# Kernel optimization log

Measured on AMD Instinct MI355X. Metric: run time of the kernel, lower is better.

The kernel has to match this reference:

```python
import jax, jax.numpy as jnp
import numpy as np

D_MODEL = 1024
NUM_HEADS = 16
HEAD_DIM = D_MODEL // NUM_HEADS
THETA = 10000.0


def _rope(x, cos, sin):
    # x: [B, H, S, hd]; cos/sin: [S, hd//2] (broadcast over B, H)
    x_even = x[..., 0::2]
    x_odd = x[..., 1::2]
    y_even = x_even * cos - x_odd * sin
    y_odd = x_even * sin + x_odd * cos
    # interleave back: stack on last dim then flatten
    y = jnp.stack((y_even, y_odd), axis=-1)
    return y.reshape(x.shape)


def setup_inputs() -> dict:
    key = jax.random.key(0)
    ks = jax.random.split(key, 5)
    B, S = 2, 2048
    x = jax.random.normal(ks[0], (B, S, D_MODEL), dtype=jnp.float32)
    scale = 1.0 / np.sqrt(D_MODEL)
    Wq = jax.random.normal(ks[1], (D_MODEL, D_MODEL), dtype=jnp.float32) * scale
    Wk = jax.random.normal(ks[2], (D_MODEL, D_MODEL), dtype=jnp.float32) * scale
    Wv = jax.random.normal(ks[3], (D_MODEL, D_MODEL), dtype=jnp.float32) * scale
    Wo = jax.random.normal(ks[4], (D_MODEL, D_MODEL), dtype=jnp.float32) * scale
    token_positions = jnp.arange(S, dtype=jnp.int64 if jax.config.jax_enable_x64 else jnp.int32)
    return {"x": x, "token_positions": token_positions, "Wq": Wq, "Wk": Wk, "Wv": Wv, "Wo": Wo}


def reference(x, token_positions, Wq, Wk, Wv, Wo):
    B, S, _ = x.shape
    # nn.Linear(d,d,bias=False): y = x @ W.T
    q = (x @ Wq.T).reshape(B, S, NUM_HEADS, HEAD_DIM).transpose(0, 2, 1, 3)
    k = (x @ Wk.T).reshape(B, S, NUM_HEADS, HEAD_DIM).transpose(0, 2, 1, 3)
    v = (x @ Wv.T).reshape(B, S, NUM_HEADS, HEAD_DIM).transpose(0, 2, 1, 3)

    # RoPE tables gathered at token_positions
    freqs = 1.0 / THETA ** (jnp.arange(0, HEAD_DIM, 2, dtype=jnp.float32) / HEAD_DIM)
    angles = token_positions.astype(jnp.float32)[:, None] * freqs[None, :]  # [S, hd//2]
    cos, sin = jnp.cos(angles), jnp.sin(angles)
    q = _rope(q, cos, sin)
    k = _rope(k, cos, sin)

    scores = jnp.einsum("bhqd,bhkd->bhqk", q, k) / np.sqrt(HEAD_DIM)
    causal = jnp.tril(jnp.ones((S, S), dtype=bool))
    scores = jnp.where(causal, scores, jnp.finfo(scores.dtype).min)
    attn = jax.nn.softmax(scores, axis=-1)
    out = jnp.einsum("bhqk,bhkd->bhqd", attn, v)  # [B,H,S,hd]
    out = out.transpose(0, 2, 1, 3).reshape(B, S, D_MODEL)
    return out @ Wo.T
```

## Files before the change

kernel.cpp:

```cpp
#include <hip/hip_runtime.h>

#define S_LEN 2048
#define NH 16
#define HD 64
#define DM 1024
#define MTOT 4096

#define QSCALE 0.18033688011112042f

typedef short bf16x8 __attribute__((ext_vector_type(8)));
typedef float f32x4 __attribute__((ext_vector_type(4)));
typedef unsigned short u16x8 __attribute__((ext_vector_type(8)));
typedef int i32x4 __attribute__((ext_vector_type(4)));

__device__ __forceinline__ unsigned short f2bf(float f) {
  unsigned int u = __builtin_bit_cast(unsigned int, f);
  u += 0x7fffu + ((u >> 16) & 1u);
  return (unsigned short)(u >> 16);
}

__device__ __forceinline__ unsigned int cvt_pk_bf16(float lo, float hi) {
  unsigned int r;
  asm("v_cvt_pk_bf16_f32 %0, %1, %2" : "=v"(r) : "v"(lo), "v"(hi));
  return r;
}

__device__ __forceinline__ void async_copy16(const void* g, void* l) {
  __builtin_amdgcn_global_load_lds(
      (const __attribute__((address_space(1))) unsigned int*)g,
      (__attribute__((address_space(3))) unsigned int*)l, 16, 0, 0);
}

__global__ void cvt_bf16_kernel(const float* __restrict__ src,
                                unsigned short* __restrict__ dst, int n) {
  int i = (blockIdx.x * 256 + threadIdx.x) * 8;
  if (i >= n) return;
  const float4* s = (const float4*)(src + i);
  float4 v0 = s[0], v1 = s[1];
  u16x8 o;
  o[0] = f2bf(v0.x); o[1] = f2bf(v0.y); o[2] = f2bf(v0.z); o[3] = f2bf(v0.w);
  o[4] = f2bf(v1.x); o[5] = f2bf(v1.y); o[6] = f2bf(v1.z); o[7] = f2bf(v1.w);
  *(u16x8*)(dst + i) = o;
}

__global__ void cvt_w_kernel(const float* __restrict__ w0, const float* __restrict__ w1,
                             const float* __restrict__ w2, const float* __restrict__ w3,
                             unsigned short* __restrict__ dst) {
  int z = blockIdx.y;
  const float* src = (z == 0) ? w0 : (z == 1) ? w1 : (z == 2) ? w2 : w3;
  int i = (blockIdx.x * 256 + threadIdx.x) * 8;
  const float4* s = (const float4*)(src + i);
  float4 v0 = s[0], v1 = s[1];
  u16x8 o;
  o[0] = f2bf(v0.x); o[1] = f2bf(v0.y); o[2] = f2bf(v0.z); o[3] = f2bf(v0.w);
  o[4] = f2bf(v1.x); o[5] = f2bf(v1.y); o[6] = f2bf(v1.z); o[7] = f2bf(v1.w);
  *(u16x8*)(dst + (size_t)z * DM * DM + i) = o;
}

__global__ void sincos_tab_kernel(const int* __restrict__ pos, float2* __restrict__ tab) {
  int idx = blockIdx.x * 256 + threadIdx.x;
  int s = idx >> 5, i = idx & 31;
  float fr = expf(-(float)i * 0.28782313662425574f);
  float ang = (float)pos[s] * fr;
  float sn, cs;
  sincosf(ang, &sn, &cs);
  tab[idx] = make_float2(cs, sn);
}

__device__ __forceinline__ void gemm_core(const unsigned short* __restrict__ A,
                                          const unsigned short* __restrict__ Bt,
                                          int m0, int n0, int K,
                                          char* a_lds, char* b_lds,
                                          f32x4 (&acc)[4][4]) {
  const int tid = threadIdx.x;
  const int w = tid >> 6, l = tid & 63;
  const int wr = w >> 1, wc = w & 1;
  const int c = l & 15, g = l >> 4;

  const size_t rs = (size_t)K * 2;
  const int lr = l >> 3;
  const int jsw = ((l & 7) ^ lr) << 4;
  const char* srcA = (const char*)A + ((size_t)m0 + w * 8 + lr) * rs + jsw;
  const char* srcB = (const char*)Bt + ((size_t)n0 + w * 8 + lr) * rs + jsw;
  char* dstA = a_lds + w * 1024 + l * 16;
  char* dstB = b_lds + w * 1024 + l * 16;
  const int csw = (c & 7) << 4;
  const int nsteps = K / 64;

  auto stage = [&](int buf, int kt) {
    const int off = buf * 16384;
#pragma unroll
    for (int i = 0; i < 4; ++i) {
      async_copy16(srcA + (size_t)i * 32 * rs + kt * 128, dstA + off + i * 4096);
      async_copy16(srcB + (size_t)i * 32 * rs + kt * 128, dstB + off + i * 4096);
    }
  };

  stage(0, 0);
  asm volatile("s_waitcnt vmcnt(0)" ::: "memory");
  __syncthreads();
  int cur = 0;

  for (int kt = 0; kt < nsteps; ++kt) {
    if (kt + 1 < nsteps) stage(cur ^ 1, kt + 1);
    const char* al = a_lds + cur * 16384;
    const char* bl = b_lds + cur * 16384;
    __builtin_amdgcn_s_setprio(1);
#pragma unroll
    for (int kk = 0; kk < 2; ++kk) {
      bf16x8 af[4], bfv[4];
#pragma unroll
      for (int mi = 0; mi < 4; ++mi)
        af[mi] = *(const bf16x8*)(al + (wr * 64 + mi * 16 + c) * 128 + ((kk * 64 + g * 16) ^ csw));
#pragma unroll
      for (int ni = 0; ni < 4; ++ni)
        bfv[ni] = *(const bf16x8*)(bl + (wc * 64 + ni * 16 + c) * 128 + ((kk * 64 + g * 16) ^ csw));
#pragma unroll
      for (int mi = 0; mi < 4; ++mi)
#pragma unroll
        for (int ni = 0; ni < 4; ++ni)
          acc[mi][ni] = __builtin_amdgcn_mfma_f32_16x16x32_bf16(af[mi], bfv[ni], acc[mi][ni], 0, 0, 0);
    }
    __builtin_amdgcn_s_setprio(0);
    asm volatile("s_waitcnt vmcnt(0)" ::: "memory");
    __syncthreads();
    cur ^= 1;
  }
}

__global__ __launch_bounds__(256)
void gemm_qkv_kernel(const unsigned short* __restrict__ X,
                     const unsigned short* __restrict__ Wq,
                     const unsigned short* __restrict__ Wk,
                     const unsigned short* __restrict__ Wv,
                     const float2* __restrict__ tab,
                     unsigned short* __restrict__ Qb,
                     unsigned short* __restrict__ Kb,
                     unsigned short* __restrict__ Vt) {
  __shared__ char a_lds[2 * 16384];
  __shared__ char b_lds[2 * 16384];
  const int z = blockIdx.z;
  const unsigned short* Bt = (z == 0) ? Wq : (z == 1) ? Wk : Wv;
  const int m0 = blockIdx.x * 128, n0 = blockIdx.y * 128;

  f32x4 acc[4][4] = {};
  gemm_core(X, Bt, m0, n0, DM, a_lds, b_lds, acc);

  const int tid = threadIdx.x;
  const int w = tid >> 6, l = tid & 63;
  const int wr = w >> 1, wc = w & 1;
  const int c = l & 15, g = l >> 4;

  if (z == 2) {
#pragma unroll
    for (int mi = 0; mi < 4; ++mi)
#pragma unroll
      for (int ni = 0; ni < 4; ++ni)
#pragma unroll
        for (int r = 0; r < 4; ++r) {
          int row = m0 + wr * 64 + mi * 16 + 4 * g + r;
          int col = n0 + wc * 64 + ni * 16 + c;
          int b = row >> 11, s = row & 2047;
          int h = col >> 6, d = col & 63;
          Vt[((size_t)(b * NH + h) * HD + d) * S_LEN + s] = f2bf(acc[mi][ni][r]);
        }
  } else {
    unsigned short* QK = z ? Kb : Qb;
    const float oscale = z ? 1.0f : QSCALE;
#pragma unroll
    for (int mi = 0; mi < 4; ++mi)
#pragma unroll
      for (int ni = 0; ni < 4; ++ni) {
        int col = n0 + wc * 64 + ni * 16 + c;
        int fi = (col >> 1) & 31;
        float sgn = (col & 1) ? 1.0f : -1.0f;
#pragma unroll
        for (int r = 0; r < 4; ++r) {
          int row = m0 + wr * 64 + mi * 16 + 4 * g + r;
          int b = row >> 11, s = row & 2047;
          float v = acc[mi][ni][r];
          float p = __shfl_xor(v, 1);
          float2 csn = tab[(s << 5) | fi];
          float vr = (v * csn.x + sgn * p * csn.y) * oscale;
          int h = col >> 6, d = col & 63;
          QK[((size_t)(b * NH + h) * S_LEN + s) * HD + d] = f2bf(vr);
        }
      }
  }
}

__global__ __launch_bounds__(256)
void gemm_out_kernel(const unsigned short* __restrict__ A,
                     const unsigned short* __restrict__ Wo,
                     float* __restrict__ out) {
  __shared__ char a_lds[2 * 16384];
  __shared__ char b_lds[2 * 16384];
  const int m0 = blockIdx.x * 128, n0 = blockIdx.y * 128;
  f32x4 acc[4][4] = {};
  gemm_core(A, Wo, m0, n0, DM, a_lds, b_lds, acc);

  const int tid = threadIdx.x;
  const int w = tid >> 6, l = tid & 63;
  const int wr = w >> 1, wc = w & 1;
  const int c = l & 15, g = l >> 4;
#pragma unroll
  for (int mi = 0; mi < 4; ++mi)
#pragma unroll
    for (int ni = 0; ni < 4; ++ni)
#pragma unroll
      for (int r = 0; r < 4; ++r) {
        int row = m0 + wr * 64 + mi * 16 + 4 * g + r;
        int col = n0 + wc * 64 + ni * 16 + c;
        out[(size_t)row * DM + col] = acc[mi][ni][r];
      }
}

__global__ __launch_bounds__(256, 4)
void attn_kernel(const unsigned short* __restrict__ Q,
                 const unsigned short* __restrict__ Kb,
                 const unsigned short* __restrict__ Vt,
                 unsigned short* __restrict__ Ob) {
  __shared__ char kbuf[2][8192];
  __shared__ char vbuf[2][8192];
  const int tid = threadIdx.x;
  const int w = tid >> 6, l = tid & 63;
  const int g = l >> 4, c = l & 15;

  const unsigned int id = blockIdx.x;
  const int bh = id & 31;
  const int j = id >> 5;
  const int a = j & 7, kk = j >> 3;
  const int qblk = (kk == 0) ? a : (kk == 1) ? (15 - a) : (kk == 2) ? (16 + a) : (31 - a);
  const int q0 = qblk * 64;

  const size_t base = (size_t)bh * (S_LEN * HD);
  const char* Kc = (const char*)(Kb + base);
  const char* Vc = (const char*)(Vt + base);

  const int lr = l >> 3;
  const int jsw = ((l & 7) << 4) ^ (lr << 4);
  const int r0 = w * 8 + lr;
  const int r1 = (4 + w) * 8 + lr;
  const char* ksrc0 = Kc + r0 * 128 + jsw;
  const char* ksrc1 = Kc + r1 * 128 + jsw;
  const char* vsrc0 = Vc + r0 * 4096 + jsw;
  const char* vsrc1 = Vc + r1 * 4096 + jsw;

  bf16x8 qf0, qf1;
  {
    const unsigned short* qp = Q + base + (size_t)(q0 + w * 16 + c) * HD + g * 8;
    qf0 = *(const bf16x8*)qp;
    qf1 = *(const bf16x8*)(qp + 32);
  }
  f32x4 oacc[4] = {};
  float rsum = 0.f;
  const int csw = (c & 7) << 4;
  const int srcA = (l & 15) | ((l & 16) << 1);
  const int srcB = srcA + 16;
  const bool hi = (l >= 32);

  auto stage = [&](int buf, int t) {
    char* kd = &kbuf[buf][w * 1024 + l * 16];
    char* vd = &vbuf[buf][w * 1024 + l * 16];
    size_t ko = (size_t)t * 8192;
    size_t vo = (size_t)t * 128;
    async_copy16(ksrc0 + ko, kd);
    async_copy16(ksrc1 + ko, kd + 4096);
    async_copy16(vsrc0 + vo, vd);
    async_copy16(vsrc1 + vo, vd + 4096);
  };

  stage(0, 0);
  asm volatile("s_waitcnt vmcnt(0)" ::: "memory");
  __syncthreads();
  int cur = 0;

  for (int t = 0; t <= qblk; ++t) {
    if (t + 1 <= qblk) stage(cur ^ 1, t + 1);
    const char* kl = kbuf[cur];
    const char* vl = vbuf[cur];
    const int kv0 = t * 64;

    f32x4 sc[4] = {};
    __builtin_amdgcn_s_setprio(1);
#pragma unroll
    for (int nt = 0; nt < 4; ++nt) {
      bf16x8 k0 = *(const bf16x8*)(kl + (nt * 16 + c) * 128 + ((g * 16) ^ csw));
      bf16x8 k1 = *(const bf16x8*)(kl + (nt * 16 + c) * 128 + ((64 + g * 16) ^ csw));
      sc[nt] = __builtin_amdgcn_mfma_f32_16x16x32_bf16(k0, qf0, sc[nt], 0, 0, 0);
      sc[nt] = __builtin_amdgcn_mfma_f32_16x16x32_bf16(k1, qf1, sc[nt], 0, 0, 0);
    }
    __builtin_amdgcn_s_setprio(0);

    if (t == qblk) {
      const int qi = q0 + w * 16 + c;
#pragma unroll
      for (int nt = 0; nt < 4; ++nt)
#pragma unroll
        for (int r = 0; r < 4; ++r) {
          int kvi = kv0 + nt * 16 + 4 * g + r;
          sc[nt][r] = exp2f((kvi > qi) ? -1e30f : sc[nt][r]);
        }
    } else {
#pragma unroll
      for (int nt = 0; nt < 4; ++nt)
#pragma unroll
        for (int r = 0; r < 4; ++r)
          sc[nt][r] = exp2f(sc[nt][r]);
    }
    unsigned int pk[4][2];
#pragma unroll
    for (int nt = 0; nt < 4; ++nt) {
      rsum += (sc[nt][0] + sc[nt][1]) + (sc[nt][2] + sc[nt][3]);
      pk[nt][0] = cvt_pk_bf16(sc[nt][0], sc[nt][1]);
      pk[nt][1] = cvt_pk_bf16(sc[nt][2], sc[nt][3]);
    }

    __builtin_amdgcn_s_setprio(1);
#pragma unroll
    for (int ks = 0; ks < 2; ++ks) {
      int a0 = __shfl((int)pk[2 * ks][0], srcA);
      int a1 = __shfl((int)pk[2 * ks][1], srcA);
      int a2 = __shfl((int)pk[2 * ks][0], srcB);
      int a3 = __shfl((int)pk[2 * ks][1], srcB);
      int b0 = __shfl((int)pk[2 * ks + 1][0], srcA);
      int b1 = __shfl((int)pk[2 * ks + 1][1], srcA);
      int b2 = __shfl((int)pk[2 * ks + 1][0], srcB);
      int b3 = __shfl((int)pk[2 * ks + 1][1], srcB);
      i32x4 pw;
      pw[0] = hi ? b0 : a0;
      pw[1] = hi ? b1 : a1;
      pw[2] = hi ? b2 : a2;
      pw[3] = hi ? b3 : a3;
      bf16x8 pf = __builtin_bit_cast(bf16x8, pw);
#pragma unroll
      for (int nt = 0; nt < 4; ++nt) {
        bf16x8 vf = *(const bf16x8*)(vl + (nt * 16 + c) * 128 + ((ks * 64 + g * 16) ^ csw));
        oacc[nt] = __builtin_amdgcn_mfma_f32_16x16x32_bf16(vf, pf, oacc[nt], 0, 0, 0);
      }
    }
    __builtin_amdgcn_s_setprio(0);

    asm volatile("s_waitcnt vmcnt(0)" ::: "memory");
    __syncthreads();
    cur ^= 1;
  }

  rsum += __shfl_xor(rsum, 16);
  rsum += __shfl_xor(rsum, 32);
  const float inv = 1.0f / rsum;

  const int b = bh >> 4, h = bh & 15;
  unsigned short* dst = Ob + ((size_t)b * S_LEN + q0 + w * 16 + c) * DM + h * HD + 4 * g;
#pragma unroll
  for (int nt = 0; nt < 4; ++nt) {
    unsigned int w0 = (unsigned int)f2bf(oacc[nt][0] * inv) | ((unsigned int)f2bf(oacc[nt][1] * inv) << 16);
    unsigned int w1 = (unsigned int)f2bf(oacc[nt][2] * inv) | ((unsigned int)f2bf(oacc[nt][3] * inv) << 16);
    uint2 pr;
    pr.x = w0;
    pr.y = w1;
    *(uint2*)(dst + nt * 16) = pr;
  }
}

extern "C" void kernel_launch(void* const* d_in, const int* in_sizes, int n_in,
                              void* d_out, int out_size, void* d_ws, size_t ws_size,
                              hipStream_t stream) {
  const float* x = (const float*)d_in[0];
  const int* tpos = (const int*)d_in[1];
  const float* wq = (const float*)d_in[2];
  const float* wk = (const float*)d_in[3];
  const float* wv = (const float*)d_in[4];
  const float* wo = (const float*)d_in[5];
  float* out = (float*)d_out;

  char* ws = (char*)d_ws;
  unsigned short* xb = (unsigned short*)(ws);
  unsigned short* wqb = (unsigned short*)(ws + 8388608);
  unsigned short* wkb = wqb + DM * DM;
  unsigned short* wvb = wqb + 2 * DM * DM;
  unsigned short* wob = wqb + 3 * DM * DM;
  unsigned short* qb = (unsigned short*)(ws + 16777216);
  unsigned short* kb = (unsigned short*)(ws + 16777216 + 8388608);
  unsigned short* vt = (unsigned short*)(ws + 16777216 + 2 * 8388608);
  unsigned short* ab = (unsigned short*)(ws + 16777216 + 3 * 8388608);
  float2* tab = (float2*)(ws + 50331648);

  cvt_bf16_kernel<<<2048, 256, 0, stream>>>(x, xb, MTOT * DM);
  cvt_w_kernel<<<dim3(512, 4), 256, 0, stream>>>(wq, wk, wv, wo, wqb);
  sincos_tab_kernel<<<256, 256, 0, stream>>>(tpos, tab);

  gemm_qkv_kernel<<<dim3(32, 8, 3), 256, 0, stream>>>(xb, wqb, wkb, wvb, tab, qb, kb, vt);
  attn_kernel<<<1024, 256, 0, stream>>>(qb, kb, vt, ab);
  gemm_out_kernel<<<dim3(32, 8), 256, 0, stream>>>(ab, wob, out);
}
```

Baseline: 127.8 us.

## Pair complementary causal query blocks per attention workgroup for balanced work

Each attention workgroup now handles two query blocks, j and 31-j, back to back, so every block walks a fixed 33 KV tiles. This balances the triangular causal workload and halves the grid to 512 blocks. The output of the first block is written mid-loop, and the K/V prefetch pipeline carries on across the switch to the second block. Launch bounds drop to 2 blocks per CU, which frees registers but lowers occupancy and leaves fewer, longer blocks.

Result: no change. 128.4 us (median of 3 runs) (+0.5%).

```diff
diff --git a/kernel.cpp b/kernel.cpp
--- a/kernel.cpp
+++ b/kernel.cpp
@@ -215,7 +215,7 @@
       }
 }
 
-__global__ __launch_bounds__(256, 4)
+__global__ __launch_bounds__(256, 2)
 void attn_kernel(const unsigned short* __restrict__ Q,
                  const unsigned short* __restrict__ Kb,
                  const unsigned short* __restrict__ Vt,
@@ -229,9 +229,7 @@
   const unsigned int id = blockIdx.x;
   const int bh = id & 31;
   const int j = id >> 5;
-  const int a = j & 7, kk = j >> 3;
-  const int qblk = (kk == 0) ? a : (kk == 1) ? (15 - a) : (kk == 2) ? (16 + a) : (31 - a);
-  const int q0 = qblk * 64;
+  const int qa = j, qb = 31 - j;
 
   const size_t base = (size_t)bh * (S_LEN * HD);
   const char* Kc = (const char*)(Kb + base);
@@ -246,9 +244,15 @@
   const char* vsrc0 = Vc + r0 * 4096 + jsw;
   const char* vsrc1 = Vc + r1 * 4096 + jsw;
 
+  const unsigned short* Qrow = Q + base + (size_t)(w * 16 + c) * HD + g * 8;
+  const int b = bh >> 4, h = bh & 15;
+  unsigned short* Obase = Ob + ((size_t)b * S_LEN + w * 16 + c) * DM + h * HD + 4 * g;
+
+  int q0 = qa * 64;
+  int qcur = qa;
   bf16x8 qf0, qf1;
   {
-    const unsigned short* qp = Q + base + (size_t)(q0 + w * 16 + c) * HD + g * 8;
+    const unsigned short* qp = Qrow + (size_t)q0 * HD;
     qf0 = *(const bf16x8*)qp;
     qf1 = *(const bf16x8*)(qp + 32);
   }
@@ -274,12 +278,14 @@
   asm volatile("s_waitcnt vmcnt(0)" ::: "memory");
   __syncthreads();
   int cur = 0;
-
-  for (int t = 0; t <= qblk; ++t) {
-    if (t + 1 <= qblk) stage(cur ^ 1, t + 1);
+  int t = 0;
+
+  for (int s = 0; s < 33; ++s) {
+    if (s < 32) stage(cur ^ 1, (t == qcur) ? 0 : t + 1);
     const char* kl = kbuf[cur];
     const char* vl = vbuf[cur];
     const int kv0 = t * 64;
+    const bool last = (t == qcur);
 
     f32x4 sc[4] = {};
     __builtin_amdgcn_s_setprio(1);
@@ -292,7 +298,7 @@
     }
     __builtin_amdgcn_s_setprio(0);
 
-    if (t == qblk) {
+    if (last) {
       const int qi = q0 + w * 16 + c;
 #pragma unroll
       for (int nt = 0; nt < 4; ++nt)
@@ -341,25 +347,38 @@
     }
     __builtin_amdgcn_s_setprio(0);
 
+    if (last) {
+      float rs = rsum;
+      rs += __shfl_xor(rs, 16);
+      rs += __shfl_xor(rs, 32);
+      const float inv = 1.0f / rs;
+      unsigned short* dst = Obase + (size_t)q0 * DM;
+#pragma unroll
+      for (int nt = 0; nt < 4; ++nt) {
+        unsigned int w0 = (unsigned int)f2bf(oacc[nt][0] * inv) | ((unsigned int)f2bf(oacc[nt][1] * inv) << 16);
+        unsigned int w1 = (unsigned int)f2bf(oacc[nt][2] * inv) | ((unsigned int)f2bf(oacc[nt][3] * inv) << 16);
+        uint2 pr;
+        pr.x = w0;
+        pr.y = w1;
+        *(uint2*)(dst + nt * 16) = pr;
+        oacc[nt] = f32x4{0.f, 0.f, 0.f, 0.f};
+      }
+      rsum = 0.f;
+      if (s < 32) {
+        q0 = qb * 64;
+        qcur = qb;
+        t = 0;
+        const unsigned short* qp = Qrow + (size_t)q0 * HD;
+        qf0 = *(const bf16x8*)qp;
+        qf1 = *(const bf16x8*)(qp + 32);
+      }
+    } else {
+      ++t;
+    }
+
     asm volatile("s_waitcnt vmcnt(0)" ::: "memory");
     __syncthreads();
     cur ^= 1;
-  }
-
-  rsum += __shfl_xor(rsum, 16);
-  rsum += __shfl_xor(rsum, 32);
-  const float inv = 1.0f / rsum;
-
-  const int b = bh >> 4, h = bh & 15;
-  unsigned short* dst = Ob + ((size_t)b * S_LEN + q0 + w * 16 + c) * DM + h * HD + 4 * g;
-#pragma unroll
-  for (int nt = 0; nt < 4; ++nt) {
-    unsigned int w0 = (unsigned int)f2bf(oacc[nt][0] * inv) | ((unsigned int)f2bf(oacc[nt][1] * inv) << 16);
-    unsigned int w1 = (unsigned int)f2bf(oacc[nt][2] * inv) | ((unsigned int)f2bf(oacc[nt][3] * inv) << 16);
-    uint2 pr;
-    pr.x = w0;
-    pr.y = w1;
-    *(uint2*)(dst + nt * 16) = pr;
   }
 }
 
@@ -391,6 +410,6 @@
   sincos_tab_kernel<<<256, 256, 0, stream>>>(tpos, tab);
 
   gemm_qkv_kernel<<<dim3(32, 8, 3), 256, 0, stream>>>(xb, wqb, wkb, wvb, tab, qb, kb, vt);
-  attn_kernel<<<1024, 256, 0, stream>>>(qb, kb, vt, ab);
+  attn_kernel<<<512, 256, 0, stream>>>(qb, kb, vt, ab);
   gemm_out_kernel<<<dim3(32, 8), 256, 0, stream>>>(ab, wob, out);
 }
```

## Pair causal query blocks per workgroup and split KV tiles across two wave groups

Applied to the files above, without the earlier changes.

The attention kernel now runs 512-thread blocks, each handling a complementary pair of query blocks (j and 31-j), so every block does the same 33 KV tiles and causal load imbalance goes away. Two wave groups take alternating KV tiles with separate double-buffered LDS, and their partial outputs and row sums are merged through LDS at the end. The risks are doubled LDS use per block, fewer blocks in flight, and extra syncs and reduction work at the epilogue.

Result: faster. 123.3 us (-3.5%).

```diff
diff --git a/kernel.cpp b/kernel.cpp
--- a/kernel.cpp
+++ b/kernel.cpp
@@ -215,23 +215,23 @@
       }
 }
 
-__global__ __launch_bounds__(256, 4)
+__global__ __launch_bounds__(512, 4)
 void attn_kernel(const unsigned short* __restrict__ Q,
                  const unsigned short* __restrict__ Kb,
                  const unsigned short* __restrict__ Vt,
                  unsigned short* __restrict__ Ob) {
-  __shared__ char kbuf[2][8192];
-  __shared__ char vbuf[2][8192];
+  __shared__ char kbuf[2][2][8192];
+  __shared__ char vbuf[2][2][8192];
   const int tid = threadIdx.x;
   const int w = tid >> 6, l = tid & 63;
+  const int G = w >> 2, ws = w & 3;
   const int g = l >> 4, c = l & 15;
 
   const unsigned int id = blockIdx.x;
   const int bh = id & 31;
   const int j = id >> 5;
-  const int a = j & 7, kk = j >> 3;
-  const int qblk = (kk == 0) ? a : (kk == 1) ? (15 - a) : (kk == 2) ? (16 + a) : (31 - a);
-  const int q0 = qblk * 64;
+  const int qa = j, qb = 31 - j;
+  const int q0a = qa * 64, q0b = qb * 64;
 
   const size_t base = (size_t)bh * (S_LEN * HD);
   const char* Kc = (const char*)(Kb + base);
@@ -239,29 +239,32 @@
 
   const int lr = l >> 3;
   const int jsw = ((l & 7) << 4) ^ (lr << 4);
-  const int r0 = w * 8 + lr;
-  const int r1 = (4 + w) * 8 + lr;
-  const char* ksrc0 = Kc + r0 * 128 + jsw;
-  const char* ksrc1 = Kc + r1 * 128 + jsw;
-  const char* vsrc0 = Vc + r0 * 4096 + jsw;
-  const char* vsrc1 = Vc + r1 * 4096 + jsw;
-
-  bf16x8 qf0, qf1;
+  const int rr0 = ws * 8 + lr;
+  const int rr1 = (4 + ws) * 8 + lr;
+  const char* ksrc0 = Kc + rr0 * 128 + jsw;
+  const char* ksrc1 = Kc + rr1 * 128 + jsw;
+  const char* vsrc0 = Vc + rr0 * 4096 + jsw;
+  const char* vsrc1 = Vc + rr1 * 4096 + jsw;
+
+  bf16x8 qfA0, qfA1, qfB0, qfB1;
   {
-    const unsigned short* qp = Q + base + (size_t)(q0 + w * 16 + c) * HD + g * 8;
-    qf0 = *(const bf16x8*)qp;
-    qf1 = *(const bf16x8*)(qp + 32);
-  }
-  f32x4 oacc[4] = {};
-  float rsum = 0.f;
+    const unsigned short* qpA = Q + base + (size_t)(q0a + ws * 16 + c) * HD + g * 8;
+    qfA0 = *(const bf16x8*)qpA;
+    qfA1 = *(const bf16x8*)(qpA + 32);
+    const unsigned short* qpB = Q + base + (size_t)(q0b + ws * 16 + c) * HD + g * 8;
+    qfB0 = *(const bf16x8*)qpB;
+    qfB1 = *(const bf16x8*)(qpB + 32);
+  }
+  f32x4 oaccA[4] = {}, oaccB[4] = {};
+  float rsA = 0.f, rsB = 0.f;
   const int csw = (c & 7) << 4;
   const int srcA = (l & 15) | ((l & 16) << 1);
   const int srcB = srcA + 16;
   const bool hi = (l >= 32);
 
   auto stage = [&](int buf, int t) {
-    char* kd = &kbuf[buf][w * 1024 + l * 16];
-    char* vd = &vbuf[buf][w * 1024 + l * 16];
+    char* kd = &kbuf[G][buf][ws * 1024 + l * 16];
+    char* vd = &vbuf[G][buf][ws * 1024 + l * 16];
     size_t ko = (size_t)t * 8192;
     size_t vo = (size_t)t * 128;
     async_copy16(ksrc0 + ko, kd);
@@ -270,30 +273,21 @@
     async_copy16(vsrc1 + vo, vd + 4096);
   };
 
-  stage(0, 0);
-  asm volatile("s_waitcnt vmcnt(0)" ::: "memory");
-  __syncthreads();
-  int cur = 0;
-
-  for (int t = 0; t <= qblk; ++t) {
-    if (t + 1 <= qblk) stage(cur ^ 1, t + 1);
-    const char* kl = kbuf[cur];
-    const char* vl = vbuf[cur];
+  auto body = [&](const char* kl, const char* vl, int q0, int qcur, int t,
+                  bf16x8 q0f, bf16x8 q1f, f32x4(&oacc)[4], float& rsum) {
     const int kv0 = t * 64;
-
     f32x4 sc[4] = {};
     __builtin_amdgcn_s_setprio(1);
 #pragma unroll
     for (int nt = 0; nt < 4; ++nt) {
       bf16x8 k0 = *(const bf16x8*)(kl + (nt * 16 + c) * 128 + ((g * 16) ^ csw));
       bf16x8 k1 = *(const bf16x8*)(kl + (nt * 16 + c) * 128 + ((64 + g * 16) ^ csw));
-      sc[nt] = __builtin_amdgcn_mfma_f32_16x16x32_bf16(k0, qf0, sc[nt], 0, 0, 0);
-      sc[nt] = __builtin_amdgcn_mfma_f32_16x16x32_bf16(k1, qf1, sc[nt], 0, 0, 0);
+      sc[nt] = __builtin_amdgcn_mfma_f32_16x16x32_bf16(k0, q0f, sc[nt], 0, 0, 0);
+      sc[nt] = __builtin_amdgcn_mfma_f32_16x16x32_bf16(k1, q1f, sc[nt], 0, 0, 0);
     }
     __builtin_amdgcn_s_setprio(0);
-
-    if (t == qblk) {
-      const int qi = q0 + w * 16 + c;
+    if (t == qcur) {
+      const int qi = q0 + ws * 16 + c;
 #pragma unroll
       for (int nt = 0; nt < 4; ++nt)
 #pragma unroll
@@ -315,7 +309,6 @@
       pk[nt][0] = cvt_pk_bf16(sc[nt][0], sc[nt][1]);
       pk[nt][1] = cvt_pk_bf16(sc[nt][2], sc[nt][3]);
     }
-
     __builtin_amdgcn_s_setprio(1);
 #pragma unroll
     for (int ks = 0; ks < 2; ++ks) {
@@ -340,26 +333,87 @@
       }
     }
     __builtin_amdgcn_s_setprio(0);
-
+  };
+
+  {
+    int t0 = (G <= qa) ? G : G - qa - 1;
+    stage(0, t0);
+  }
+  asm volatile("s_waitcnt vmcnt(0)" ::: "memory");
+  __syncthreads();
+  int cur = 0;
+
+  for (int s = 0; s < 17; ++s) {
+    const int i = 2 * s + G;
+    const int inext = i + 2;
+    if (inext <= 32) {
+      int tn = (inext <= qa) ? inext : inext - qa - 1;
+      stage(cur ^ 1, tn);
+    }
+    if (i <= 32) {
+      const char* kl = kbuf[G][cur];
+      const char* vl = vbuf[G][cur];
+      if (i <= qa)
+        body(kl, vl, q0a, qa, i, qfA0, qfA1, oaccA, rsA);
+      else
+        body(kl, vl, q0b, qb, i - qa - 1, qfB0, qfB1, oaccB, rsB);
+    }
     asm volatile("s_waitcnt vmcnt(0)" ::: "memory");
     __syncthreads();
     cur ^= 1;
   }
 
-  rsum += __shfl_xor(rsum, 16);
-  rsum += __shfl_xor(rsum, 32);
-  const float inv = 1.0f / rsum;
-
+  rsA += __shfl_xor(rsA, 16);
+  rsA += __shfl_xor(rsA, 32);
+  rsB += __shfl_xor(rsB, 16);
+  rsB += __shfl_xor(rsB, 32);
+  float* lf = (float*)&kbuf[0][0][0];
+  float* lrs = (float*)&vbuf[0][0][0];
+  const int row = ws * 16 + c;
   const int b = bh >> 4, h = bh & 15;
-  unsigned short* dst = Ob + ((size_t)b * S_LEN + q0 + w * 16 + c) * DM + h * HD + 4 * g;
-#pragma unroll
-  for (int nt = 0; nt < 4; ++nt) {
-    unsigned int w0 = (unsigned int)f2bf(oacc[nt][0] * inv) | ((unsigned int)f2bf(oacc[nt][1] * inv) << 16);
-    unsigned int w1 = (unsigned int)f2bf(oacc[nt][2] * inv) | ((unsigned int)f2bf(oacc[nt][3] * inv) << 16);
-    uint2 pr;
-    pr.x = w0;
-    pr.y = w1;
-    *(uint2*)(dst + nt * 16) = pr;
+
+  if (G == 1) {
+#pragma unroll
+    for (int nt = 0; nt < 4; ++nt)
+      *(f32x4*)(lf + row * 64 + nt * 16 + 4 * g) = oaccA[nt];
+    if (g == 0) lrs[row] = rsA;
+  }
+  __syncthreads();
+  if (G == 0) {
+    float inv = 1.0f / (rsA + lrs[row]);
+    unsigned short* dst = Ob + ((size_t)b * S_LEN + q0a + row) * DM + h * HD + 4 * g;
+#pragma unroll
+    for (int nt = 0; nt < 4; ++nt) {
+      f32x4 o = oaccA[nt] + *(f32x4*)(lf + row * 64 + nt * 16 + 4 * g);
+      unsigned int w0 = (unsigned int)f2bf(o[0] * inv) | ((unsigned int)f2bf(o[1] * inv) << 16);
+      unsigned int w1 = (unsigned int)f2bf(o[2] * inv) | ((unsigned int)f2bf(o[3] * inv) << 16);
+      uint2 pr;
+      pr.x = w0;
+      pr.y = w1;
+      *(uint2*)(dst + nt * 16) = pr;
+    }
+  }
+  __syncthreads();
+  if (G == 0) {
+#pragma unroll
+    for (int nt = 0; nt < 4; ++nt)
+      *(f32x4*)(lf + row * 64 + nt * 16 + 4 * g) = oaccB[nt];
+    if (g == 0) lrs[row] = rsB;
+  }
+  __syncthreads();
+  if (G == 1) {
+    float inv = 1.0f / (rsB + lrs[row]);
+    unsigned short* dst = Ob + ((size_t)b * S_LEN + q0b + row) * DM + h * HD + 4 * g;
+#pragma unroll
+    for (int nt = 0; nt < 4; ++nt) {
+      f32x4 o = oaccB[nt] + *(f32x4*)(lf + row * 64 + nt * 16 + 4 * g);
+      unsigned int w0 = (unsigned int)f2bf(o[0] * inv) | ((unsigned int)f2bf(o[1] * inv) << 16);
+      unsigned int w1 = (unsigned int)f2bf(o[2] * inv) | ((unsigned int)f2bf(o[3] * inv) << 16);
+      uint2 pr;
+      pr.x = w0;
+      pr.y = w1;
+      *(uint2*)(dst + nt * 16) = pr;
+    }
   }
 }
 
@@ -391,6 +445,6 @@
   sincos_tab_kernel<<<256, 256, 0, stream>>>(tpos, tab);
 
   gemm_qkv_kernel<<<dim3(32, 8, 3), 256, 0, stream>>>(xb, wqb, wkb, wvb, tab, qb, kb, vt);
-  attn_kernel<<<1024, 256, 0, stream>>>(qb, kb, vt, ab);
+  attn_kernel<<<512, 512, 0, stream>>>(qb, kb, vt, ab);
   gemm_out_kernel<<<dim3(32, 8), 256, 0, stream>>>(ab, wob, out);
 }
```
